# Kernel tuning notes

Hardware: AMD Instinct MI355X
Metric: run time of the kernel (lower is better)

## Reference

```python
import jax, jax.numpy as jnp
import numpy as np

IN_F, OUT_F, R = 4096, 4096, 16
ALPHA = 32.0
SCALING = ALPHA / R


def setup_inputs() -> dict:
    key = jax.random.key(0)
    kx, kw, ka = jax.random.split(key, 3)
    x = jax.random.normal(kx, (4, 2048, IN_F), dtype=jnp.float32)
    # xavier_normal for weight: std = sqrt(2/(fan_in+fan_out))
    std = float(np.sqrt(2.0 / (IN_F + OUT_F)))
    weight = jax.random.normal(kw, (OUT_F, IN_F), dtype=jnp.float32) * std
    bias = jnp.zeros((OUT_F,), dtype=jnp.float32)
    A = jax.random.normal(ka, (R, IN_F), dtype=jnp.float32) * 0.01
    # B initialized to zeros in the module, but use small random values so the
    # LoRA path is numerically exercised for kernel correctness testing.
    B = jax.random.normal(jax.random.fold_in(key, 7), (OUT_F, R), dtype=jnp.float32) * 0.01
    return {"x": x, "weight": weight, "bias": bias, "A": A, "B": B}


def reference(x, weight, bias, A, B):
    # out = x @ W^T + bias + scaling * ((x @ A^T) @ B^T)
    out = jnp.einsum('bsi,oi->bso', x, weight) + bias
    xa = jnp.einsum('bsi,ri->bsr', x, A)           # [b, s, r] low-rank projection
    out = out + SCALING * jnp.einsum('bsr,or->bso', xa, B)
    return out
```

## Files before the change

### kernel.cpp

```cpp
#include <hip/hip_runtime.h>
#include <hip/hip_bf16.h>
#include <cstdint>
#include <cstddef>


#define IN_F   4096
#define OUT_F  4096
#define MROWS  8192
#define RLORA  16
#define LORA_SCALE 2.0f

#define BM 128
#define BN 128
#define BK 32

#define CAST_BLOCKS 32768
#define FOLD_BLOCKS 4096

typedef __bf16 bf16x8 __attribute__((ext_vector_type(8)));
typedef float  f32x4  __attribute__((ext_vector_type(4)));

__device__ __forceinline__ unsigned short f2bf_rne(float f) {
    union { float f; unsigned u; } v; v.f = f;
    unsigned u = v.u;
    return (unsigned short)((u + 0x7FFFu + ((u >> 16) & 1u)) >> 16);
}

__device__ __forceinline__ void gl_lds16(const unsigned short* g, unsigned short* l) {
    __builtin_amdgcn_global_load_lds(
        (const __attribute__((address_space(1))) unsigned int*)g,
        (__attribute__((address_space(3))) unsigned int*)l,
        16, 0, 0);
}


__global__ void prep_kernel(const float* __restrict__ x,
                            const float* __restrict__ W,
                            const float* __restrict__ A,
                            const float* __restrict__ B,
                            unsigned short* __restrict__ xb,
                            unsigned short* __restrict__ wb) {
    __shared__ float sB[RLORA];
    const int bid = blockIdx.x;
    if (bid < CAST_BLOCKS) {
        int i = bid * blockDim.x + threadIdx.x;
        float4 v = ((const float4*)x)[i];
        ushort4 o;
        o.x = f2bf_rne(v.x); o.y = f2bf_rne(v.y);
        o.z = f2bf_rne(v.z); o.w = f2bf_rne(v.w);
        ((ushort4*)xb)[i] = o;
    } else {
        const int o = bid - CAST_BLOCKS;
        if (threadIdx.x < RLORA) sB[threadIdx.x] = B[o * RLORA + threadIdx.x];
        __syncthreads();
        const float4* W4  = (const float4*)(W + (size_t)o * IN_F);
        ushort4*      Wp4 = (ushort4*)(wb + (size_t)o * IN_F);
        for (int i4 = threadIdx.x; i4 < IN_F / 4; i4 += blockDim.x) {
            float4 w = W4[i4];
            float ax = 0.f, ay = 0.f, az = 0.f, aw = 0.f;
            #pragma unroll
            for (int r = 0; r < RLORA; ++r) {
                float4 a = ((const float4*)(A + (size_t)r * IN_F))[i4];
                float s = sB[r];
                ax += s * a.x; ay += s * a.y; az += s * a.z; aw += s * a.w;
            }
            w.x += LORA_SCALE * ax; w.y += LORA_SCALE * ay;
            w.z += LORA_SCALE * az; w.w += LORA_SCALE * aw;
            ushort4 ov;
            ov.x = f2bf_rne(w.x); ov.y = f2bf_rne(w.y);
            ov.z = f2bf_rne(w.z); ov.w = f2bf_rne(w.w);
            Wp4[i4] = ov;
        }
    }
}


__global__ __launch_bounds__(256)
void gemm_bt_bias(const unsigned short* __restrict__ Xb,
                  const unsigned short* __restrict__ Wb,
                  const float* __restrict__ bias,
                  float* __restrict__ out) {
    __shared__ __align__(16) unsigned short As[BM * BK];
    __shared__ __align__(16) unsigned short Bs[BN * BK];

    const int tid  = threadIdx.x;
    const int wave = tid >> 6;
    const int lane = tid & 63;
    const int quad = lane >> 4;
    const int r16  = lane & 15;
    const int wm   = wave >> 1;
    const int wn   = wave & 1;

    const int bid = blockIdx.x;
    const int xcd = bid & 7;
    const int t   = bid >> 3;
    const int n0  = ((xcd << 2) | (t & 3)) * BN;
    const int m0  = (t >> 2) * BM;

    const int c0   = wave * 128 + lane;
    const int c1   = c0 + 64;
    const int row0 = c0 >> 2, kc0 = c0 & 3;
    const int row1 = c1 >> 2, kc1 = c1 & 3;

    const unsigned short* gA0 = Xb + (size_t)(m0 + row0) * IN_F + kc0 * 8;
    const unsigned short* gA1 = Xb + (size_t)(m0 + row1) * IN_F + kc1 * 8;
    const unsigned short* gB0 = Wb + (size_t)(n0 + row0) * IN_F + kc0 * 8;
    const unsigned short* gB1 = Wb + (size_t)(n0 + row1) * IN_F + kc1 * 8;

    unsigned short* lA0 = As + (wave * 128 +  0) * 8;
    unsigned short* lA1 = As + (wave * 128 + 64) * 8;
    unsigned short* lB0 = Bs + (wave * 128 +  0) * 8;
    unsigned short* lB1 = Bs + (wave * 128 + 64) * 8;

    const unsigned short* pA = As + ((wm * 64 + r16) * BK) + quad * 8;
    const unsigned short* pB = Bs + ((wn * 64 + r16) * BK) + quad * 8;

    f32x4 acc[4][4] = {};

    for (int k0 = 0; k0 < IN_F; k0 += BK) {
        gl_lds16(gA0, lA0);
        gl_lds16(gA1, lA1);
        gl_lds16(gB0, lB0);
        gl_lds16(gB1, lB1);
        gA0 += BK; gA1 += BK; gB0 += BK; gB1 += BK;
        __syncthreads();

        bf16x8 aF[4], bF[4];
        #pragma unroll
        for (int mi = 0; mi < 4; ++mi)
            aF[mi] = *(const bf16x8*)(pA + mi * 16 * BK);
        #pragma unroll
        for (int ni = 0; ni < 4; ++ni)
            bF[ni] = *(const bf16x8*)(pB + ni * 16 * BK);

        #pragma unroll
        for (int mi = 0; mi < 4; ++mi)
            #pragma unroll
            for (int ni = 0; ni < 4; ++ni)
                acc[mi][ni] = __builtin_amdgcn_mfma_f32_16x16x32_bf16(
                    aF[mi], bF[ni], acc[mi][ni], 0, 0, 0);

        __syncthreads();
    }

    float bv[4];
    #pragma unroll
    for (int ni = 0; ni < 4; ++ni)
        bv[ni] = bias[n0 + wn * 64 + ni * 16 + r16];

    #pragma unroll
    for (int mi = 0; mi < 4; ++mi) {
        #pragma unroll
        for (int i = 0; i < 4; ++i) {
            int mg = m0 + wm * 64 + mi * 16 + quad * 4 + i;
            float* orow = out + (size_t)mg * OUT_F + (n0 + wn * 64 + r16);
            #pragma unroll
            for (int ni = 0; ni < 4; ++ni)
                orow[ni * 16] = acc[mi][ni][i] + bv[ni];
        }
    }
}


extern "C" void kernel_launch(void* const* d_in, const int* in_sizes, int n_in,
                              void* d_out, int out_size, void* d_ws, size_t ws_size,
                              hipStream_t stream) {
    const float* x    = (const float*)d_in[0];
    const float* W    = (const float*)d_in[1];
    const float* bias = (const float*)d_in[2];
    const float* A    = (const float*)d_in[3];
    const float* B    = (const float*)d_in[4];
    float* out = (float*)d_out;

    unsigned short* xb = (unsigned short*)d_ws;
    unsigned short* wb = xb + (size_t)MROWS * IN_F;

    prep_kernel<<<CAST_BLOCKS + FOLD_BLOCKS, 256, 0, stream>>>(x, W, A, B, xb, wb);
    gemm_bt_bias<<<2048, 256, 0, stream>>>(xb, wb, bias, out);
}
```

Measured before the change: 606.6 us.

## Enlarge GEMM tiles to 256x256 with 4-stage LDS pipeline and swizzle

The bf16 GEMM goes from 128x128 tiles with 256 threads to 256x256 tiles with 512 threads, so each wave computes a 128x64 sub-tile. It adds a 4-buffer LDS ring with three K-slices prefetched ahead. Global-to-LDS loads are tracked with explicit vmcnt waits and raw s_barrier calls instead of two __syncthreads per step. An XOR swizzle on the K-chunk index is meant to avoid LDS bank conflicts, and inline ds_read_b128 with split lgkmcnt waits and setprio lets MFMAs start before all fragments arrive. The 128KB of LDS limits occupancy to one block per CU, and the hand-counted waits are fragile.

After: 531.1 us. 12.4% less time.

```diff
diff --git a/kernel.cpp b/kernel.cpp
--- a/kernel.cpp
+++ b/kernel.cpp
@@ -10,15 +10,17 @@
 #define RLORA  16
 #define LORA_SCALE 2.0f
 
-#define BM 128
-#define BN 128
-#define BK 32
-
 #define CAST_BLOCKS 32768
 #define FOLD_BLOCKS 4096
 
+#define BM   256
+#define BN   256
+#define BKT  32
+#define NT   (IN_F / BKT)
+
 typedef __bf16 bf16x8 __attribute__((ext_vector_type(8)));
 typedef float  f32x4  __attribute__((ext_vector_type(4)));
+typedef int    i32x4  __attribute__((ext_vector_type(4)));
 
 __device__ __forceinline__ unsigned short f2bf_rne(float f) {
     union { float f; unsigned u; } v; v.f = f;
@@ -75,88 +77,130 @@
 }
 
 
-__global__ __launch_bounds__(256)
+__global__ __launch_bounds__(512, 2)
 void gemm_bt_bias(const unsigned short* __restrict__ Xb,
                   const unsigned short* __restrict__ Wb,
                   const float* __restrict__ bias,
                   float* __restrict__ out) {
-    __shared__ __align__(16) unsigned short As[BM * BK];
-    __shared__ __align__(16) unsigned short Bs[BN * BK];
+    __shared__ __align__(16) unsigned short smem[4 * 16384];
 
     const int tid  = threadIdx.x;
     const int wave = tid >> 6;
     const int lane = tid & 63;
     const int quad = lane >> 4;
     const int r16  = lane & 15;
-    const int wm   = wave >> 1;
-    const int wn   = wave & 1;
+    const int wm   = wave >> 2;
+    const int wn   = wave & 3;
 
     const int bid = blockIdx.x;
     const int xcd = bid & 7;
     const int t   = bid >> 3;
-    const int n0  = ((xcd << 2) | (t & 3)) * BN;
-    const int m0  = (t >> 2) * BM;
-
-    const int c0   = wave * 128 + lane;
-    const int c1   = c0 + 64;
-    const int row0 = c0 >> 2, kc0 = c0 & 3;
-    const int row1 = c1 >> 2, kc1 = c1 & 3;
-
-    const unsigned short* gA0 = Xb + (size_t)(m0 + row0) * IN_F + kc0 * 8;
-    const unsigned short* gA1 = Xb + (size_t)(m0 + row1) * IN_F + kc1 * 8;
-    const unsigned short* gB0 = Wb + (size_t)(n0 + row0) * IN_F + kc0 * 8;
-    const unsigned short* gB1 = Wb + (size_t)(n0 + row1) * IN_F + kc1 * 8;
-
-    unsigned short* lA0 = As + (wave * 128 +  0) * 8;
-    unsigned short* lA1 = As + (wave * 128 + 64) * 8;
-    unsigned short* lB0 = Bs + (wave * 128 +  0) * 8;
-    unsigned short* lB1 = Bs + (wave * 128 + 64) * 8;
-
-    const unsigned short* pA = As + ((wm * 64 + r16) * BK) + quad * 8;
-    const unsigned short* pB = Bs + ((wn * 64 + r16) * BK) + quad * 8;
-
-    f32x4 acc[4][4] = {};
-
-    for (int k0 = 0; k0 < IN_F; k0 += BK) {
-        gl_lds16(gA0, lA0);
-        gl_lds16(gA1, lA1);
-        gl_lds16(gB0, lB0);
-        gl_lds16(gB1, lB1);
-        gA0 += BK; gA1 += BK; gB0 += BK; gB1 += BK;
-        __syncthreads();
-
-        bf16x8 aF[4], bF[4];
+    const int n0  = (xcd * 2 + (t & 1)) * BN;
+    const int m0  = (t >> 1) * BM;
+
+    const int qA0 = wave * 128 + lane;
+    const int qA1 = qA0 + 64;
+    const int rA0 = qA0 >> 2, kA0 = (qA0 & 3) ^ ((rA0 >> 1) & 3);
+    const int rA1 = qA1 >> 2, kA1 = (qA1 & 3) ^ ((rA1 >> 1) & 3);
+
+    const unsigned short* gA0 = Xb + (size_t)(m0 + rA0) * IN_F + kA0 * 8;
+    const unsigned short* gA1 = Xb + (size_t)(m0 + rA1) * IN_F + kA1 * 8;
+    const unsigned short* gB0 = Wb + (size_t)(n0 + rA0) * IN_F + kA0 * 8;
+    const unsigned short* gB1 = Wb + (size_t)(n0 + rA1) * IN_F + kA1 * 8;
+
+    const unsigned dA0 = wave * 1024;
+    const unsigned dA1 = dA0 + 512;
+    const unsigned dB0 = 8192 + wave * 1024;
+    const unsigned dB1 = dB0 + 512;
+
+    const unsigned slot  = (unsigned)(quad ^ ((r16 >> 1) & 3));
+    const unsigned aoff  = (unsigned)((wm * 128 + r16) * 64) + slot * 16;
+    const unsigned boff  = 16384u + (unsigned)((wn * 64 + r16) * 64) + slot * 16;
+    const unsigned sbase = (unsigned)(size_t)
+        ((__attribute__((address_space(3))) unsigned short*)smem);
+
+    f32x4 acc[8][4] = {};
+
+    #pragma unroll
+    for (int s = 0; s < 3; ++s) {
+        unsigned short* Lb = smem + (s << 14);
+        gl_lds16(gA0, Lb + dA0); gl_lds16(gA1, Lb + dA1);
+        gl_lds16(gB0, Lb + dB0); gl_lds16(gB1, Lb + dB1);
+        gA0 += BKT; gA1 += BKT; gB0 += BKT; gB1 += BKT;
+    }
+    asm volatile("s_waitcnt vmcnt(8)" ::: "memory");
+    __builtin_amdgcn_s_barrier();
+
+    for (int p = 0; p < NT; ++p) {
+        if (p + 3 < NT) {
+            unsigned short* Lb = smem + (((p + 3) & 3) << 14);
+            gl_lds16(gA0, Lb + dA0); gl_lds16(gA1, Lb + dA1);
+            gl_lds16(gB0, Lb + dB0); gl_lds16(gB1, Lb + dB1);
+            gA0 += BKT; gA1 += BKT; gB0 += BKT; gB1 += BKT;
+        }
+
+        const unsigned bufb = sbase + ((unsigned)(p & 3) << 15);
+        const unsigned ab = bufb + aoff;
+        const unsigned bb = bufb + boff;
+
+        i32x4 aR[8]; i32x4 bR[4];
+        asm volatile("ds_read_b128 %0, %1"             : "=v"(bR[0]) : "v"(bb));
+        asm volatile("ds_read_b128 %0, %1 offset:1024" : "=v"(bR[1]) : "v"(bb));
+        asm volatile("ds_read_b128 %0, %1 offset:2048" : "=v"(bR[2]) : "v"(bb));
+        asm volatile("ds_read_b128 %0, %1 offset:3072" : "=v"(bR[3]) : "v"(bb));
+        asm volatile("ds_read_b128 %0, %1"             : "=v"(aR[0]) : "v"(ab));
+        asm volatile("ds_read_b128 %0, %1 offset:1024" : "=v"(aR[1]) : "v"(ab));
+        asm volatile("ds_read_b128 %0, %1 offset:2048" : "=v"(aR[2]) : "v"(ab));
+        asm volatile("ds_read_b128 %0, %1 offset:3072" : "=v"(aR[3]) : "v"(ab));
+        asm volatile("ds_read_b128 %0, %1 offset:4096" : "=v"(aR[4]) : "v"(ab));
+        asm volatile("ds_read_b128 %0, %1 offset:5120" : "=v"(aR[5]) : "v"(ab));
+        asm volatile("ds_read_b128 %0, %1 offset:6144" : "=v"(aR[6]) : "v"(ab));
+        asm volatile("ds_read_b128 %0, %1 offset:7168" : "=v"(aR[7]) : "v"(ab));
+
+        asm volatile("s_waitcnt lgkmcnt(4)" ::: "memory");
+        __builtin_amdgcn_sched_barrier(0);
+        __builtin_amdgcn_s_setprio(1);
         #pragma unroll
-        for (int mi = 0; mi < 4; ++mi)
-            aF[mi] = *(const bf16x8*)(pA + mi * 16 * BK);
+        for (int mi = 0; mi < 4; ++mi) {
+            const bf16x8 a = __builtin_bit_cast(bf16x8, aR[mi]);
+            #pragma unroll
+            for (int nj = 0; nj < 4; ++nj)
+                acc[mi][nj] = __builtin_amdgcn_mfma_f32_16x16x32_bf16(
+                    a, __builtin_bit_cast(bf16x8, bR[nj]), acc[mi][nj], 0, 0, 0);
+        }
+        asm volatile("s_waitcnt lgkmcnt(0)" ::: "memory");
+        __builtin_amdgcn_sched_barrier(0);
         #pragma unroll
-        for (int ni = 0; ni < 4; ++ni)
-            bF[ni] = *(const bf16x8*)(pB + ni * 16 * BK);
-
-        #pragma unroll
-        for (int mi = 0; mi < 4; ++mi)
-            #pragma unroll
-            for (int ni = 0; ni < 4; ++ni)
-                acc[mi][ni] = __builtin_amdgcn_mfma_f32_16x16x32_bf16(
-                    aF[mi], bF[ni], acc[mi][ni], 0, 0, 0);
-
-        __syncthreads();
+        for (int mi = 4; mi < 8; ++mi) {
+            const bf16x8 a = __builtin_bit_cast(bf16x8, aR[mi]);
+            #pragma unroll
+            for (int nj = 0; nj < 4; ++nj)
+                acc[mi][nj] = __builtin_amdgcn_mfma_f32_16x16x32_bf16(
+                    a, __builtin_bit_cast(bf16x8, bR[nj]), acc[mi][nj], 0, 0, 0);
+        }
+        __builtin_amdgcn_sched_barrier(0);
+        __builtin_amdgcn_s_setprio(0);
+
+        if (p + 3 < NT)       { asm volatile("s_waitcnt vmcnt(8)" ::: "memory"); }
+        else if (p + 3 == NT) { asm volatile("s_waitcnt vmcnt(4)" ::: "memory"); }
+        else                  { asm volatile("s_waitcnt vmcnt(0)" ::: "memory"); }
+        __builtin_amdgcn_s_barrier();
     }
 
     float bv[4];
     #pragma unroll
-    for (int ni = 0; ni < 4; ++ni)
-        bv[ni] = bias[n0 + wn * 64 + ni * 16 + r16];
+    for (int nj = 0; nj < 4; ++nj)
+        bv[nj] = bias[n0 + wn * 64 + nj * 16 + r16];
 
     #pragma unroll
-    for (int mi = 0; mi < 4; ++mi) {
+    for (int mi = 0; mi < 8; ++mi) {
         #pragma unroll
         for (int i = 0; i < 4; ++i) {
-            int mg = m0 + wm * 64 + mi * 16 + quad * 4 + i;
+            const int mg = m0 + wm * 128 + mi * 16 + quad * 4 + i;
             float* orow = out + (size_t)mg * OUT_F + (n0 + wn * 64 + r16);
             #pragma unroll
-            for (int ni = 0; ni < 4; ++ni)
-                orow[ni * 16] = acc[mi][ni][i] + bv[ni];
+            for (int nj = 0; nj < 4; ++nj)
+                orow[nj * 16] = acc[mi][nj][i] + bv[nj];
         }
     }
 }
@@ -176,5 +220,5 @@
     unsigned short* wb = xb + (size_t)MROWS * IN_F;
 
     prep_kernel<<<CAST_BLOCKS + FOLD_BLOCKS, 256, 0, stream>>>(x, W, A, B, xb, wb);
-    gemm_bt_bias<<<2048, 256, 0, stream>>>(xb, wb, bias, out);
-}
+    gemm_bt_bias<<<(MROWS / BM) * (OUT_F / BN), 512, 0, stream>>>(xb, wb, bias, out);
+}
```
